# Kernel tuning notes

Hardware: AMD Instinct MI355X
Metric: run time of the kernel (lower is better)

The kernel has to match this reference:

```python
import jax, jax.numpy as jnp
import numpy as np

WS = 14          # window size
NH = 12          # num heads
C = 768          # hidden dim
HD = C // NH     # head dim = 64
MLP = 3072       # mlp dim
EPS = 1e-6


def _layernorm(x, g, b):
    mu = jnp.mean(x, axis=-1, keepdims=True)
    var = jnp.mean(jnp.square(x - mu), axis=-1, keepdims=True)
    return (x - mu) * jax.lax.rsqrt(var + EPS) * g + b


def setup_inputs() -> dict:
    key = jax.random.key(0)
    ks = jax.random.split(key, 8)
    B, H, W = 8, 64, 64
    f32 = jnp.float32
    d = {}
    d["x"] = jax.random.normal(ks[0], (B, H, W, C), f32)
    d["ln1_g"] = jnp.ones((C,), f32)
    d["ln1_b"] = jnp.zeros((C,), f32)
    d["qkv_w"] = (jax.random.normal(ks[1], (C, 3 * C), f32) * 0.02)
    d["qkv_b"] = jnp.zeros((3 * C,), f32)
    d["proj_w"] = (jax.random.normal(ks[2], (C, C), f32) * 0.02)
    d["proj_b"] = jnp.zeros((C,), f32)
    d["rel_pos_h"] = (jax.random.normal(ks[3], (2 * WS - 1, HD), f32) * 0.02)
    d["rel_pos_w"] = (jax.random.normal(ks[4], (2 * WS - 1, HD), f32) * 0.02)
    d["ln2_g"] = jnp.ones((C,), f32)
    d["ln2_b"] = jnp.zeros((C,), f32)
    d["mlp_w1"] = (jax.random.normal(ks[5], (C, MLP), f32) * 0.02)
    d["mlp_b1"] = jnp.zeros((MLP,), f32)
    d["mlp_w2"] = (jax.random.normal(ks[6], (MLP, C), f32) * 0.02)
    d["mlp_b2"] = jnp.zeros((C,), f32)
    return d


def reference(x, ln1_g, ln1_b, qkv_w, qkv_b, proj_w, proj_b,
              rel_pos_h, rel_pos_w, ln2_g, ln2_b,
              mlp_w1, mlp_b1, mlp_w2, mlp_b2):
    B, H, W, _ = x.shape
    xn = _layernorm(x, ln1_g, ln1_b)

    # ---- window partition (pad to multiple of WS) ----
    pad_h = (-H) % WS
    pad_w = (-W) % WS
    Hp, Wp = H + pad_h, W + pad_w
    xp = jnp.pad(xn, ((0, 0), (0, pad_h), (0, pad_w), (0, 0)))
    # [B, Hp/WS, WS, Wp/WS, WS, C] -> [Bn, WS, WS, C]
    win = xp.reshape(B, Hp // WS, WS, Wp // WS, WS, C)
    win = win.transpose(0, 1, 3, 2, 4, 5).reshape(-1, WS, WS, C)
    Bn = win.shape[0]
    N = WS * WS

    # ---- attention with decomposed relative position bias ----
    qkv = win.reshape(Bn, N, C) @ qkv_w + qkv_b                 # [Bn, N, 3C]
    qkv = qkv.reshape(Bn, N, 3, NH, HD).transpose(2, 0, 3, 1, 4)
    qkv = qkv.reshape(3, Bn * NH, N, HD)
    q, k, v = qkv[0], qkv[1], qkv[2]

    scale = HD ** -0.5
    attn = jnp.einsum('bnd,bmd->bnm', q * scale, k)             # [Bn*NH, N, N]

    # rel coords: q_size == k_size == WS, rel_pos already has 2*WS-1 rows
    coords = jnp.arange(WS)[:, None] - jnp.arange(WS)[None, :] + (WS - 1)
    Rh = rel_pos_h[coords]                                      # [WS, WS, HD]
    Rw = rel_pos_w[coords]                                      # [WS, WS, HD]
    rq = q.reshape(Bn * NH, WS, WS, HD)
    rel_h = jnp.einsum('bhwc,hkc->bhwk', rq, Rh)                # [B', WS, WS, WS]
    rel_w = jnp.einsum('bhwc,wkc->bhwk', rq, Rw)
    attn = (attn.reshape(Bn * NH, WS, WS, WS, WS)
            + rel_h[:, :, :, :, None]
            + rel_w[:, :, :, None, :]).reshape(Bn * NH, N, N)

    attn = jax.nn.softmax(attn, axis=-1)
    out = jnp.einsum('bnm,bmd->bnd', attn, v)                   # [Bn*NH, N, HD]
    out = out.reshape(Bn, NH, WS, WS, HD).transpose(0, 2, 3, 1, 4).reshape(Bn, WS, WS, C)
    out = out @ proj_w + proj_b

    # ---- window unpartition ----
    out = out.reshape(B, Hp // WS, Wp // WS, WS, WS, C)
    out = out.transpose(0, 1, 3, 2, 4, 5).reshape(B, Hp, Wp, C)[:, :H, :W, :]

    x1 = x + out
    y = _layernorm(x1, ln2_g, ln2_b)
    y = jax.nn.gelu(y @ mlp_w1 + mlp_b1, approximate=False) @ mlp_w2 + mlp_b2
    return x1 + y
```

## Files before the change

kernel.cpp:

```cpp
#include <hip/hip_runtime.h>
#include <hip/hip_bf16.h>
#include <cstdint>
#include <cstddef>

using bf16 = __hip_bfloat16;
typedef __attribute__((ext_vector_type(8))) short short8;
typedef __attribute__((ext_vector_type(4))) float f32x4;

typedef __attribute__((address_space(1))) const void as1_void;
typedef __attribute__((address_space(3))) void as3_void;

__device__ __forceinline__ f32x4 mfma16x16x32(short8 a, short8 b, f32x4 c) {
  return __builtin_amdgcn_mfma_f32_16x16x32_bf16(a, b, c, 0, 0, 0);
}

__device__ __forceinline__ void gload_lds16(const void* g, void* l) {
  __builtin_amdgcn_global_load_lds((as1_void*)g, (as3_void*)l, 16, 0, 0);
}

__device__ __forceinline__ uint32_t cvtpk(float a, float b) {
  uint32_t r;
  asm("v_cvt_pk_bf16_f32 %0, %1, %2" : "=v"(r) : "v"(a), "v"(b));
  return r;
}

__device__ __forceinline__ void vmwait4() { asm volatile("s_waitcnt vmcnt(4)" ::: "memory"); }
__device__ __forceinline__ void vmwait0() { asm volatile("s_waitcnt vmcnt(0)" ::: "memory"); }

__device__ __forceinline__ float gelu_f(float v) {
  const float u = 0.7978845608f * v * (1.f + 0.044715f * v * v);
  const float e = __expf(-2.f * fabsf(u));
  const float t = (1.f - e) / (1.f + e);
  return 0.5f * v * (1.f + (u < 0.f ? -t : t));
}

static constexpr int MROWS = 39200;
static constexpr int MPAD  = 39296;
static constexpr int TOK2  = 32768;

__global__ __launch_bounds__(256)
void transpose_cast(const float* __restrict__ in, bf16* __restrict__ out, int K, int N) {
  __shared__ float t[32][33];
  const int tx = threadIdx.x & 31, ty = threadIdx.x >> 5;
  const int bx = blockIdx.x, by = blockIdx.y;
  const int x = bx * 32 + tx;
  for (int r = ty; r < 32; r += 8)
    t[r][tx] = in[(size_t)(by * 32 + r) * N + x];
  __syncthreads();
  const int xo = by * 32 + tx;
  for (int r = ty; r < 32; r += 8)
    out[(size_t)(bx * 32 + r) * K + xo] = __float2bfloat16(t[tx][r]);
}

__global__ __launch_bounds__(256)
void ln1_partition(const float* __restrict__ x, const float* __restrict__ g,
                   const float* __restrict__ bb, bf16* __restrict__ out) {
  const int token = blockIdx.x * 4 + (threadIdx.x >> 6);
  const int lane = threadIdx.x & 63;
  const int win = token / 196, tok = token % 196;
  const int b_ = win / 25, wh = (win / 5) % 5, ww = win % 5;
  const int i = tok / 14, j = tok % 14;
  const int h = wh * 14 + i, w = ww * 14 + j;
  bf16* o = out + (size_t)token * 768;
  if (h >= 64 || w >= 64) {
    for (int t = 0; t < 12; ++t) o[lane + 64 * t] = __float2bfloat16(0.f);
    return;
  }
  const float* src = x + ((size_t)((b_ * 64 + h) * 64 + w)) * 768;
  float vals[12], s = 0.f, ss = 0.f;
  #pragma unroll
  for (int t = 0; t < 12; ++t) {
    float v = src[lane + 64 * t];
    vals[t] = v; s += v; ss += v * v;
  }
  #pragma unroll
  for (int d = 32; d > 0; d >>= 1) { s += __shfl_xor(s, d); ss += __shfl_xor(ss, d); }
  const float mu = s * (1.f / 768.f);
  const float var = ss * (1.f / 768.f) - mu * mu;
  const float inv = rsqrtf(var + 1e-6f);
  #pragma unroll
  for (int t = 0; t < 12; ++t) {
    const int c = lane + 64 * t;
    o[c] = __float2bfloat16((vals[t] - mu) * inv * g[c] + bb[c]);
  }
}

__global__ __launch_bounds__(256)
void ln2_kernel(const float* __restrict__ x1, const float* __restrict__ g,
                const float* __restrict__ bb, bf16* __restrict__ out) {
  const int token = blockIdx.x * 4 + (threadIdx.x >> 6);
  const int lane = threadIdx.x & 63;
  const float* src = x1 + (size_t)token * 768;
  bf16* o = out + (size_t)token * 768;
  float vals[12], s = 0.f, ss = 0.f;
  #pragma unroll
  for (int t = 0; t < 12; ++t) {
    float v = src[lane + 64 * t];
    vals[t] = v; s += v; ss += v * v;
  }
  #pragma unroll
  for (int d = 32; d > 0; d >>= 1) { s += __shfl_xor(s, d); ss += __shfl_xor(ss, d); }
  const float mu = s * (1.f / 768.f);
  const float var = ss * (1.f / 768.f) - mu * mu;
  const float inv = rsqrtf(var + 1e-6f);
  #pragma unroll
  for (int t = 0; t < 12; ++t) {
    const int c = lane + 64 * t;
    o[c] = __float2bfloat16((vals[t] - mu) * inv * g[c] + bb[c]);
  }
}

template<int EPI>
__global__ __launch_bounds__(256)
void gemm_bf16(const bf16* __restrict__ A, const bf16* __restrict__ Bt,
               const float* __restrict__ bias, int K, int Mreal,
               const float* __restrict__ fin, float* __restrict__ fout,
               bf16* __restrict__ ob0, bf16* __restrict__ ob1, bf16* __restrict__ ob2) {
  __shared__ __align__(16) bf16 SMEM[16384];
  bf16* const lA0 = SMEM;
  bf16* const lA1 = SMEM + 4096;
  bf16* const lB0 = SMEM + 8192;
  bf16* const lB1 = SMEM + 12288;
  const int tid = threadIdx.x;
  const int lane = tid & 63, wv = tid >> 6;
  const int lr = lane & 15, hi = lane >> 4;
  const int wm = wv >> 1, wn = wv & 1;

  const int gx = gridDim.x;
  const int nwg = gx * gridDim.y;
  int lin = blockIdx.y * gx + blockIdx.x;
  {
    const int q8 = nwg >> 3, r8 = nwg & 7;
    const int xcd = lin & 7, pos = lin >> 3;
    lin = (xcd < r8 ? xcd * (q8 + 1) : r8 * (q8 + 1) + (xcd - r8) * q8) + pos;
  }
  const size_t arow0 = (size_t)(lin / gx) * 128;
  const size_t brow0 = (size_t)(lin % gx) * 128;
  f32x4 acc[4][4] = {};

  auto stage = [&](bf16* bufA, bf16* bufB, int kt) {
    const int k0 = kt * 32;
    #pragma unroll
    for (int it = 0; it < 2; ++it) {
      const int seg = it * 256 + tid;
      const int row = seg >> 2, kq = seg & 3;
      const size_t dst = (size_t)(it * 256 + wv * 64) * 8;
      if constexpr (EPI == 1) {
        const int k = k0 + kq * 8;
        gload_lds16(A + ((size_t)(k >> 6) * MPAD + arow0 + row) * 64 + (k & 63), bufA + dst);
      } else {
        gload_lds16(A + (arow0 + row) * K + k0 + kq * 8, bufA + dst);
      }
      gload_lds16(Bt + (brow0 + row) * K + k0 + kq * 8, bufB + dst);
    }
  };
  auto compute = [&](const bf16* bufA, const bf16* bufB) {
    short8 af[4], bfr[4];
    #pragma unroll
    for (int m = 0; m < 4; ++m) af[m] = *(const short8*)&bufA[(wm * 64 + m * 16 + lr) * 32 + hi * 8];
    #pragma unroll
    for (int n = 0; n < 4; ++n) bfr[n] = *(const short8*)&bufB[(wn * 64 + n * 16 + lr) * 32 + hi * 8];
    #pragma unroll
    for (int m = 0; m < 4; ++m)
      #pragma unroll
      for (int n = 0; n < 4; ++n)
        acc[m][n] = mfma16x16x32(af[m], bfr[n], acc[m][n]);
  };

  const int nt = K >> 5;
  stage(lA0, lB0, 0);
  stage(lA1, lB1, 1);
  for (int t = 0; t < nt; t += 2) {
    vmwait4();
    __builtin_amdgcn_s_barrier();
    __builtin_amdgcn_sched_barrier(0);
    compute(lA0, lB0);
    __builtin_amdgcn_sched_barrier(0);
    __builtin_amdgcn_s_barrier();
    if (t + 2 < nt) { stage(lA0, lB0, t + 2); vmwait4(); }
    else            { vmwait0(); }
    __builtin_amdgcn_s_barrier();
    __builtin_amdgcn_sched_barrier(0);
    compute(lA1, lB1);
    __builtin_amdgcn_sched_barrier(0);
    __builtin_amdgcn_s_barrier();
    if (t + 3 < nt) stage(lA1, lB1, t + 3);
  }

  if constexpr (EPI == 0 || EPI == 2) {
    bf16* ct = SMEM;
    #pragma unroll
    for (int n = 0; n < 4; ++n) {
      const int col = wn * 64 + n * 16 + lr;
      const float bv = bias[(int)brow0 + col];
      #pragma unroll
      for (int m = 0; m < 4; ++m) {
        #pragma unroll
        for (int e = 0; e < 4; ++e) {
          const int row = wm * 64 + m * 16 + hi * 4 + e;
          float v = acc[m][n][e] + bv;
          if constexpr (EPI == 2) v = gelu_f(v);
          const int byte = (row << 8) + (col << 1);
          *(bf16*)((char*)ct + (byte ^ ((row & 7) << 5))) = __float2bfloat16(v);
        }
      }
    }
    __syncthreads();
    #pragma unroll
    for (int i = 0; i < 8; ++i) {
      const int lin16 = i * 256 + tid;
      const int row = lin16 >> 4;
      const int u   = lin16 & 15;
      const int byte = (row << 8) + (u << 4);
      const short8 val = *(const short8*)((char*)ct + (byte ^ ((row & 7) << 5)));
      const int grow = (int)arow0 + row;
      const int gcol = (int)brow0 + u * 8;
      if constexpr (EPI == 0) {
        if (grow < Mreal) {
          const int which = gcol / 768, head = (gcol >> 6) % 12, d = gcol & 63;
          bf16* dstb = (which == 0) ? ob0 : ((which == 1) ? ob1 : ob2);
          *(short8*)&dstb[((size_t)head * MPAD + grow) * 64 + d] = val;
        }
      } else {
        *(short8*)&ob0[(size_t)grow * 3072 + gcol] = val;
      }
    }
  } else {
    #pragma unroll
    for (int n = 0; n < 4; ++n) {
      const int col = (int)brow0 + wn * 64 + n * 16 + lr;
      const float bv = bias[col];
      #pragma unroll
      for (int m = 0; m < 4; ++m) {
        #pragma unroll
        for (int e = 0; e < 4; ++e) {
          const int row = (int)arow0 + wm * 64 + m * 16 + hi * 4 + e;
          const float v = acc[m][n][e] + bv;
          if constexpr (EPI == 1) {
            if (row < Mreal) {
              const int win = row / 196, tok = row % 196;
              const int b_ = win / 25, wh = (win / 5) % 5, ww = win % 5;
              const int i = tok / 14, j = tok % 14;
              const int h = wh * 14 + i, w = ww * 14 + j;
              if (h < 64 && w < 64) {
                const size_t idx = ((size_t)((b_ * 64 + h) * 64 + w)) * 768 + col;
                fout[idx] = fin[idx] + v;
              }
            }
          } else {
            const size_t idx = (size_t)row * 768 + col;
            fout[idx] = fin[idx] + v;
          }
        }
      }
    }
  }
}

__global__ __launch_bounds__(256)
void attn_kernel(const bf16* __restrict__ qb, const bf16* __restrict__ kb,
                 const bf16* __restrict__ vb, const float* __restrict__ rph,
                 const float* __restrict__ rpw, bf16* __restrict__ aout) {
  __shared__ __align__(16) char SM[65248];
  bf16* pbh    = (bf16*)SM;
  bf16* pbw    = (bf16*)(SM + 4096);
  bf16* Gh     = (bf16*)(SM + 8192);
  bf16* Gw     = (bf16*)(SM + 23168);
  char* klds   = SM;
  char* vtb    = SM + 25600;
  bf16* relh_s = (bf16*)(SM + 54272);
  bf16* relw_s = (bf16*)(SM + 59760);

  const int bh = blockIdx.x;
  const int win = bh / 12, head = bh % 12;
  const size_t base = ((size_t)head * MPAD + win * 196) * 64;
  const bf16* Q  = qb + base;
  const bf16* Kp = kb + base;
  const bf16* Vp = vb + base;
  const int tid = threadIdx.x, lane = tid & 63, wv = tid >> 6;
  const int lr = lane & 15, hi = lane >> 4;

  for (int i = tid; i < 32 * 64; i += 256) {
    const int r = i >> 6, c = i & 63;
    const bool ok = r < 27;
    pbh[i] = __float2bfloat16(ok ? rph[r * 64 + c] : 0.f);
    pbw[i] = __float2bfloat16(ok ? rpw[r * 64 + c] : 0.f);
  }
  __syncthreads();
  {
    short8 bh00 = *(const short8*)&pbh[(lr) * 64 + hi * 8];
    short8 bh01 = *(const short8*)&pbh[(lr) * 64 + 32 + hi * 8];
    short8 bh10 = *(const short8*)&pbh[(16 + lr) * 64 + hi * 8];
    short8 bh11 = *(const short8*)&pbh[(16 + lr) * 64 + 32 + hi * 8];
    short8 bw00 = *(const short8*)&pbw[(lr) * 64 + hi * 8];
    short8 bw01 = *(const short8*)&pbw[(lr) * 64 + 32 + hi * 8];
    short8 bw10 = *(const short8*)&pbw[(16 + lr) * 64 + hi * 8];
    short8 bw11 = *(const short8*)&pbw[(16 + lr) * 64 + 32 + hi * 8];
    for (int mt = wv; mt < 13; mt += 4) {
      const short8 a0 = *(const short8*)&Q[(mt * 16 + lr) * 64 + hi * 8];
      const short8 a1 = *(const short8*)&Q[(mt * 16 + lr) * 64 + 32 + hi * 8];
      f32x4 g0 = {}, g1 = {}, g2 = {}, g3 = {};
      g0 = mfma16x16x32(a0, bh00, g0); g0 = mfma16x16x32(a1, bh01, g0);
      g1 = mfma16x16x32(a0, bh10, g1); g1 = mfma16x16x32(a1, bh11, g1);
      g2 = mfma16x16x32(a0, bw00, g2); g2 = mfma16x16x32(a1, bw01, g2);
      g3 = mfma16x16x32(a0, bw10, g3); g3 = mfma16x16x32(a1, bw11, g3);
      #pragma unroll
      for (int e = 0; e < 4; ++e) {
        const int row = mt * 16 + hi * 4 + e;
        Gh[row * 36 + lr]      = __float2bfloat16(g0[e]);
        Gh[row * 36 + 16 + lr] = __float2bfloat16(g1[e]);
        Gw[row * 36 + lr]      = __float2bfloat16(g2[e]);
        Gw[row * 36 + 16 + lr] = __float2bfloat16(g3[e]);
      }
    }
  }
  __syncthreads();
  bf16 ghr[11], gwr[11];
  #pragma unroll
  for (int t = 0; t < 11; ++t) {
    const int i = tid + t * 256;
    if (i < 196 * 14) {
      const int q = i / 14, kk = i - (i / 14) * 14;
      const int rh = q / 14 - kk + 13;
      const int rw2 = q - (q / 14) * 14 - kk + 13;
      ghr[t] = Gh[q * 36 + rh];
      gwr[t] = Gw[q * 36 + rw2];
    }
  }
  __syncthreads();
  #pragma unroll
  for (int t = 0; t < 11; ++t) {
    const int i = tid + t * 256;
    if (i < 196 * 14) { relh_s[i] = ghr[t]; relw_s[i] = gwr[t]; }
  }
  for (int c = wv; c < 25; c += 4) {
    const int row = c * 8 + (lane >> 3);
    const int ch  = (lane & 7) ^ (row & 7);
    gload_lds16(Kp + row * 64 + ch * 8, klds + c * 1024);
  }
  for (int i = tid; i < 196 * 8; i += 256) {
    const int key = i >> 3, dg = (i & 7) * 8;
    const short8 v = *(const short8*)&Vp[key * 64 + dg];
    #pragma unroll
    for (int j = 0; j < 8; ++j) {
      const int idx = (dg + j) * 448 + key * 2;
      *(bf16*)(vtb + (idx ^ (j << 4))) = ((const bf16*)&v)[j];
    }
  }
  for (int i = tid; i < 64 * 28; i += 256) {
    const int d = i / 28, key = 196 + i - (i / 28) * 28;
    const int idx = d * 448 + key * 2;
    *(bf16*)(vtb + (idx ^ ((d & 7) << 4))) = __float2bfloat16(0.f);
  }
  __syncthreads();

  for (int qt = wv; qt < 13; qt += 4) {
    const int q = qt * 16 + lr;
    const int qc = q < 196 ? q : 195;
    const short8 bq0 = *(const short8*)&Q[(qt * 16 + lr) * 64 + hi * 8];
    const short8 bq1 = *(const short8*)&Q[(qt * 16 + lr) * 64 + 32 + hi * 8];
    f32x4 s[13];
    __builtin_amdgcn_s_setprio(1);
    #pragma unroll
    for (int nt = 0; nt < 13; ++nt) {
      const int key = nt * 16 + lr;
      const char* kr = klds + key * 128;
      const short8 ka0 = *(const short8*)(kr + (((hi) ^ (key & 7)) << 4));
      const short8 ka1 = *(const short8*)(kr + (((hi + 4) ^ (key & 7)) << 4));
      f32x4 z = {};
      z = mfma16x16x32(ka0, bq0, z);
      z = mfma16x16x32(ka1, bq1, z);
      s[nt] = z;
    }
    __builtin_amdgcn_s_setprio(0);
    float mx = -3.0e38f;
    #pragma unroll
    for (int nt = 0; nt < 13; ++nt) {
      #pragma unroll
      for (int e = 0; e < 4; ++e) {
        const int key = nt * 16 + hi * 4 + e;
        const int kh = key / 14, kw = key - kh * 14;
        float v = s[nt][e] * 0.125f + __bfloat162float(relh_s[qc * 14 + kh])
                                    + __bfloat162float(relw_s[qc * 14 + kw]);
        v = (key < 196) ? v : -3.0e38f;
        s[nt][e] = v;
        mx = fmaxf(mx, v);
      }
    }
    mx = fmaxf(mx, __shfl_xor(mx, 16));
    mx = fmaxf(mx, __shfl_xor(mx, 32));
    float sm = 0.f;
    #pragma unroll
    for (int nt = 0; nt < 13; ++nt)
      #pragma unroll
      for (int e = 0; e < 4; ++e) {
        const float p = __expf(s[nt][e] - mx);
        s[nt][e] = p; sm += p;
      }
    sm += __shfl_xor(sm, 16);
    sm += __shfl_xor(sm, 32);
    const float rinv = 1.f / sm;
    f32x4 o[4] = {};
    #pragma unroll
    for (int kk = 0; kk < 7; ++kk) {
      const uint32_t x0 = cvtpk(s[2 * kk][0] * rinv, s[2 * kk][1] * rinv);
      const uint32_t x1 = cvtpk(s[2 * kk][2] * rinv, s[2 * kk][3] * rinv);
      const uint32_t y0 = cvtpk(s[2 * kk + 1][0] * rinv, s[2 * kk + 1][1] * rinv);
      const uint32_t y1 = cvtpk(s[2 * kk + 1][2] * rinv, s[2 * kk + 1][3] * rinv);
      const uint32_t s0 = (hi < 2) ? y0 : x0, s1 = (hi < 2) ? y1 : x1;
      const uint32_t t0 = __shfl_xor(s0, 32), t1 = __shfl_xor(s1, 32);
      const uint32_t o0 = (hi < 2) ? x0 : y0, o1 = (hi < 2) ? x1 : y1;
      const bool sendOwn = (hi == 1) || (hi == 2);
      const uint32_t u0 = sendOwn ? o0 : t0, u1 = sendOwn ? o1 : t1;
      const uint32_t r0 = __shfl_xor(u0, 16), r1 = __shfl_xor(u1, 16);
      union { uint32_t u[4]; short8 v; } pf;
      pf.u[0] = (hi == 0) ? x0 : ((hi == 2) ? t0 : r0);
      pf.u[1] = (hi == 0) ? x1 : ((hi == 2) ? t1 : r1);
      pf.u[2] = (hi == 3) ? y0 : ((hi == 1) ? t0 : r0);
      pf.u[3] = (hi == 3) ? y1 : ((hi == 1) ? t1 : r1);
      __builtin_amdgcn_s_setprio(1);
      #pragma unroll
      for (int n2 = 0; n2 < 4; ++n2) {
        const int d = n2 * 16 + lr;
        const int idx = d * 448 + (kk * 32 + hi * 8) * 2;
        const short8 va = *(const short8*)(vtb + (idx ^ ((lr & 7) << 4)));
        o[n2] = mfma16x16x32(va, pf.v, o[n2]);
      }
      __builtin_amdgcn_s_setprio(0);
    }
    if (q < 196) {
      bf16* orow = aout + ((size_t)head * MPAD + win * 196 + q) * 64;
      #pragma unroll
      for (int n2 = 0; n2 < 4; ++n2) {
        uint32_t d0 = cvtpk(o[n2][0], o[n2][1]);
        uint32_t d1 = cvtpk(o[n2][2], o[n2][3]);
        uint32_t* dst = (uint32_t*)&orow[n2 * 16 + hi * 4];
        dst[0] = d0; dst[1] = d1;
      }
    }
  }
}

extern "C" void kernel_launch(void* const* d_in, const int* in_sizes, int n_in,
                              void* d_out, int out_size, void* d_ws, size_t ws_size,
                              hipStream_t stream) {
  (void)in_sizes; (void)n_in; (void)out_size; (void)ws_size;
  const float* x      = (const float*)d_in[0];
  const float* ln1_g  = (const float*)d_in[1];
  const float* ln1_b  = (const float*)d_in[2];
  const float* qkv_w  = (const float*)d_in[3];
  const float* qkv_b  = (const float*)d_in[4];
  const float* proj_w = (const float*)d_in[5];
  const float* proj_b = (const float*)d_in[6];
  const float* rph    = (const float*)d_in[7];
  const float* rpw    = (const float*)d_in[8];
  const float* ln2_g  = (const float*)d_in[9];
  const float* ln2_b  = (const float*)d_in[10];
  const float* w1     = (const float*)d_in[11];
  const float* b1v    = (const float*)d_in[12];
  const float* w2     = (const float*)d_in[13];
  const float* b2v    = (const float*)d_in[14];
  float* outp = (float*)d_out;

  char* ws = (char*)d_ws;
  size_t off = 0;
  auto alloc = [&](size_t bytes) { char* p = ws + off; off += (bytes + 255) & ~(size_t)255; return p; };
  bf16* qkv_wt  = (bf16*)alloc((size_t)2304 * 768 * 2);
  bf16* proj_wt = (bf16*)alloc((size_t)768 * 768 * 2);
  bf16* w1t     = (bf16*)alloc((size_t)3072 * 768 * 2);
  bf16* w2t     = (bf16*)alloc((size_t)768 * 3072 * 2);
  const size_t szB1 = (size_t)MPAD * 768 * 2;
  const size_t szB2 = (size_t)TOK2 * 768 * 2;
  char* regB = alloc(szB1 > szB2 ? szB1 : szB2);
  const size_t szQKV = (size_t)3 * 12 * MPAD * 64 * 2;
  const size_t szH   = (size_t)TOK2 * 3072 * 2;
  char* regC = alloc(szQKV > szH ? szQKV : szH);

  bf16* xnwin   = (bf16*)regB;
  bf16* attnout = (bf16*)regB;
  bf16* xn2     = (bf16*)regB;
  bf16* qbuf    = (bf16*)regC;
  bf16* kbuf    = qbuf + (size_t)12 * MPAD * 64;
  bf16* vbuf    = kbuf + (size_t)12 * MPAD * 64;
  bf16* hbuf    = (bf16*)regC;

  transpose_cast<<<dim3(2304 / 32, 768 / 32), 256, 0, stream>>>(qkv_w, qkv_wt, 768, 2304);
  transpose_cast<<<dim3(768 / 32, 768 / 32), 256, 0, stream>>>(proj_w, proj_wt, 768, 768);
  transpose_cast<<<dim3(3072 / 32, 768 / 32), 256, 0, stream>>>(w1, w1t, 768, 3072);
  transpose_cast<<<dim3(768 / 32, 3072 / 32), 256, 0, stream>>>(w2, w2t, 3072, 768);

  ln1_partition<<<dim3(MROWS / 4), 256, 0, stream>>>(x, ln1_g, ln1_b, xnwin);

  gemm_bf16<0><<<dim3(2304 / 128, MPAD / 128), 256, 0, stream>>>(
      xnwin, qkv_wt, qkv_b, 768, MROWS, nullptr, nullptr, qbuf, kbuf, vbuf);

  attn_kernel<<<dim3(2400), 256, 0, stream>>>(qbuf, kbuf, vbuf, rph, rpw, attnout);

  gemm_bf16<1><<<dim3(768 / 128, MPAD / 128), 256, 0, stream>>>(
      attnout, proj_wt, proj_b, 768, MROWS, x, outp, nullptr, nullptr, nullptr);

  ln2_kernel<<<dim3(TOK2 / 4), 256, 0, stream>>>(outp, ln2_g, ln2_b, xn2);

  gemm_bf16<2><<<dim3(3072 / 128, TOK2 / 128), 256, 0, stream>>>(
      xn2, w1t, b1v, 768, TOK2, nullptr, nullptr, hbuf, nullptr, nullptr);
  gemm_bf16<3><<<dim3(768 / 128, TOK2 / 128), 256, 0, stream>>>(
      hbuf, w2t, b2v, 3072, TOK2, outp, outp, nullptr, nullptr, nullptr);
}
```

Baseline: 1.140 ms.

## Write V transposed from QKV GEMM and read K/V directly in attention

The QKV GEMM epilogue now writes V in a head-major, d-major (transposed) layout. The attention kernel therefore drops its LDS staging of K and the LDS transpose of V, and reads both straight from global memory. That cuts attention LDS use and raises the occupancy hint to 3 blocks per CU, at the cost of uncoalesced per-lane global reads inside the MFMA loops. Separately, the GEMM main loop replaces the hand-scheduled double-buffer waits and barriers with a simpler stage-ahead pattern using __syncthreads. That may reduce how well loads overlap with MFMA work.

```diff
diff --git a/kernel.cpp b/kernel.cpp
--- a/kernel.cpp
+++ b/kernel.cpp
@@ -23,9 +23,6 @@
   asm("v_cvt_pk_bf16_f32 %0, %1, %2" : "=v"(r) : "v"(a), "v"(b));
   return r;
 }
-
-__device__ __forceinline__ void vmwait4() { asm volatile("s_waitcnt vmcnt(4)" ::: "memory"); }
-__device__ __forceinline__ void vmwait0() { asm volatile("s_waitcnt vmcnt(0)" ::: "memory"); }
 
 __device__ __forceinline__ float gelu_f(float v) {
   const float u = 0.7978845608f * v * (1.f + 0.044715f * v * v);
@@ -169,22 +166,14 @@
 
   const int nt = K >> 5;
   stage(lA0, lB0, 0);
-  stage(lA1, lB1, 1);
+  __syncthreads();
   for (int t = 0; t < nt; t += 2) {
-    vmwait4();
-    __builtin_amdgcn_s_barrier();
-    __builtin_amdgcn_sched_barrier(0);
+    if (t + 1 < nt) stage(lA1, lB1, t + 1);
     compute(lA0, lB0);
-    __builtin_amdgcn_sched_barrier(0);
-    __builtin_amdgcn_s_barrier();
-    if (t + 2 < nt) { stage(lA0, lB0, t + 2); vmwait4(); }
-    else            { vmwait0(); }
-    __builtin_amdgcn_s_barrier();
-    __builtin_amdgcn_sched_barrier(0);
+    __syncthreads();
+    if (t + 2 < nt) stage(lA0, lB0, t + 2);
     compute(lA1, lB1);
-    __builtin_amdgcn_sched_barrier(0);
-    __builtin_amdgcn_s_barrier();
-    if (t + 3 < nt) stage(lA1, lB1, t + 3);
+    __syncthreads();
   }
 
   if constexpr (EPI == 0 || EPI == 2) {
@@ -206,23 +195,50 @@
       }
     }
     __syncthreads();
-    #pragma unroll
-    for (int i = 0; i < 8; ++i) {
-      const int lin16 = i * 256 + tid;
-      const int row = lin16 >> 4;
-      const int u   = lin16 & 15;
-      const int byte = (row << 8) + (u << 4);
-      const short8 val = *(const short8*)((char*)ct + (byte ^ ((row & 7) << 5)));
-      const int grow = (int)arow0 + row;
-      const int gcol = (int)brow0 + u * 8;
-      if constexpr (EPI == 0) {
-        if (grow < Mreal) {
-          const int which = gcol / 768, head = (gcol >> 6) % 12, d = gcol & 63;
-          bf16* dstb = (which == 0) ? ob0 : ((which == 1) ? ob1 : ob2);
-          *(short8*)&dstb[((size_t)head * MPAD + grow) * 64 + d] = val;
+    if constexpr (EPI == 0) {
+      if ((int)brow0 >= 1536) {
+        const int head_base = ((int)brow0 >> 6) % 12;
+        #pragma unroll
+        for (int i = 0; i < 8; ++i) {
+          const int idx = i * 256 + tid;
+          const int dl = idx >> 4;
+          const int h2 = dl >> 6, d = dl & 63;
+          const int tg = (idx & 15) * 8;
+          union { bf16 h[8]; short8 v; } u8;
+          #pragma unroll
+          for (int j = 0; j < 8; ++j) {
+            const int tok = tg + j;
+            const int byte = (tok << 8) + (dl << 1);
+            u8.h[j] = *(const bf16*)((const char*)ct + (byte ^ ((tok & 7) << 5)));
+          }
+          *(short8*)&ob2[((size_t)(head_base + h2) * 64 + d) * MPAD + arow0 + tg] = u8.v;
         }
       } else {
-        *(short8*)&ob0[(size_t)grow * 3072 + gcol] = val;
+        #pragma unroll
+        for (int i = 0; i < 8; ++i) {
+          const int lin16 = i * 256 + tid;
+          const int row = lin16 >> 4;
+          const int u   = lin16 & 15;
+          const int byte = (row << 8) + (u << 4);
+          const short8 val = *(const short8*)((char*)ct + (byte ^ ((row & 7) << 5)));
+          const int grow = (int)arow0 + row;
+          const int gcol = (int)brow0 + u * 8;
+          if (grow < Mreal) {
+            const int which = gcol / 768, head = (gcol >> 6) % 12, d = gcol & 63;
+            bf16* dstb = (which == 0) ? ob0 : ob1;
+            *(short8*)&dstb[((size_t)head * MPAD + grow) * 64 + d] = val;
+          }
+        }
+      }
+    } else {
+      #pragma unroll
+      for (int i = 0; i < 8; ++i) {
+        const int lin16 = i * 256 + tid;
+        const int row = lin16 >> 4;
+        const int u   = lin16 & 15;
+        const int byte = (row << 8) + (u << 4);
+        const short8 val = *(const short8*)((char*)ct + (byte ^ ((row & 7) << 5)));
+        *(short8*)&ob0[(size_t)((int)arow0 + row) * 3072 + (int)brow0 + u * 8] = val;
       }
     }
   } else {
@@ -257,26 +273,24 @@
   }
 }
 
-__global__ __launch_bounds__(256)
+__global__ __launch_bounds__(256, 3)
 void attn_kernel(const bf16* __restrict__ qb, const bf16* __restrict__ kb,
-                 const bf16* __restrict__ vb, const float* __restrict__ rph,
+                 const bf16* __restrict__ vtg_all, const float* __restrict__ rph,
                  const float* __restrict__ rpw, bf16* __restrict__ aout) {
-  __shared__ __align__(16) char SM[65248];
+  __shared__ __align__(16) char SM[38144];
   bf16* pbh    = (bf16*)SM;
   bf16* pbw    = (bf16*)(SM + 4096);
   bf16* Gh     = (bf16*)(SM + 8192);
   bf16* Gw     = (bf16*)(SM + 23168);
-  char* klds   = SM;
-  char* vtb    = SM + 25600;
-  bf16* relh_s = (bf16*)(SM + 54272);
-  bf16* relw_s = (bf16*)(SM + 59760);
+  bf16* relh_s = (bf16*)SM;
+  bf16* relw_s = (bf16*)(SM + 5488);
 
   const int bh = blockIdx.x;
   const int win = bh / 12, head = bh % 12;
   const size_t base = ((size_t)head * MPAD + win * 196) * 64;
-  const bf16* Q  = qb + base;
-  const bf16* Kp = kb + base;
-  const bf16* Vp = vb + base;
+  const bf16* Q   = qb + base;
+  const bf16* Kp  = kb + base;
+  const bf16* Vt  = vtg_all + (size_t)head * 64 * MPAD + win * 196;
   const int tid = threadIdx.x, lane = tid & 63, wv = tid >> 6;
   const int lr = lane & 15, hi = lane >> 4;
 
@@ -333,25 +347,6 @@
     const int i = tid + t * 256;
     if (i < 196 * 14) { relh_s[i] = ghr[t]; relw_s[i] = gwr[t]; }
   }
-  for (int c = wv; c < 25; c += 4) {
-    const int row = c * 8 + (lane >> 3);
-    const int ch  = (lane & 7) ^ (row & 7);
-    gload_lds16(Kp + row * 64 + ch * 8, klds + c * 1024);
-  }
-  for (int i = tid; i < 196 * 8; i += 256) {
-    const int key = i >> 3, dg = (i & 7) * 8;
-    const short8 v = *(const short8*)&Vp[key * 64 + dg];
-    #pragma unroll
-    for (int j = 0; j < 8; ++j) {
-      const int idx = (dg + j) * 448 + key * 2;
-      *(bf16*)(vtb + (idx ^ (j << 4))) = ((const bf16*)&v)[j];
-    }
-  }
-  for (int i = tid; i < 64 * 28; i += 256) {
-    const int d = i / 28, key = 196 + i - (i / 28) * 28;
-    const int idx = d * 448 + key * 2;
-    *(bf16*)(vtb + (idx ^ ((d & 7) << 4))) = __float2bfloat16(0.f);
-  }
   __syncthreads();
 
   for (int qt = wv; qt < 13; qt += 4) {
@@ -359,14 +354,13 @@
     const int qc = q < 196 ? q : 195;
     const short8 bq0 = *(const short8*)&Q[(qt * 16 + lr) * 64 + hi * 8];
     const short8 bq1 = *(const short8*)&Q[(qt * 16 + lr) * 64 + 32 + hi * 8];
-    f32x4 s[13];
+    f32x4 s[14];
     __builtin_amdgcn_s_setprio(1);
     #pragma unroll
     for (int nt = 0; nt < 13; ++nt) {
       const int key = nt * 16 + lr;
-      const char* kr = klds + key * 128;
-      const short8 ka0 = *(const short8*)(kr + (((hi) ^ (key & 7)) << 4));
-      const short8 ka1 = *(const short8*)(kr + (((hi + 4) ^ (key & 7)) << 4));
+      const short8 ka0 = *(const short8*)&Kp[key * 64 + hi * 8];
+      const short8 ka1 = *(const short8*)&Kp[key * 64 + 32 + hi * 8];
       f32x4 z = {};
       z = mfma16x16x32(ka0, bq0, z);
       z = mfma16x16x32(ka1, bq1, z);
@@ -400,6 +394,7 @@
     sm += __shfl_xor(sm, 16);
     sm += __shfl_xor(sm, 32);
     const float rinv = 1.f / sm;
+    s[13] = f32x4{0.f, 0.f, 0.f, 0.f};
     f32x4 o[4] = {};
     #pragma unroll
     for (int kk = 0; kk < 7; ++kk) {
@@ -422,8 +417,7 @@
       #pragma unroll
       for (int n2 = 0; n2 < 4; ++n2) {
         const int d = n2 * 16 + lr;
-        const int idx = d * 448 + (kk * 32 + hi * 8) * 2;
-        const short8 va = *(const short8*)(vtb + (idx ^ ((lr & 7) << 4)));
+        const short8 va = *(const short8*)&Vt[(size_t)d * MPAD + kk * 32 + hi * 8];
         o[n2] = mfma16x16x32(va, pf.v, o[n2]);
       }
       __builtin_amdgcn_s_setprio(0);
@@ -481,7 +475,7 @@
   bf16* xn2     = (bf16*)regB;
   bf16* qbuf    = (bf16*)regC;
   bf16* kbuf    = qbuf + (size_t)12 * MPAD * 64;
-  bf16* vbuf    = kbuf + (size_t)12 * MPAD * 64;
+  bf16* vbuf_t  = kbuf + (size_t)12 * MPAD * 64;
   bf16* hbuf    = (bf16*)regC;
 
   transpose_cast<<<dim3(2304 / 32, 768 / 32), 256, 0, stream>>>(qkv_w, qkv_wt, 768, 2304);
@@ -492,9 +486,9 @@
   ln1_partition<<<dim3(MROWS / 4), 256, 0, stream>>>(x, ln1_g, ln1_b, xnwin);
 
   gemm_bf16<0><<<dim3(2304 / 128, MPAD / 128), 256, 0, stream>>>(
-      xnwin, qkv_wt, qkv_b, 768, MROWS, nullptr, nullptr, qbuf, kbuf, vbuf);
-
-  attn_kernel<<<dim3(2400), 256, 0, stream>>>(qbuf, kbuf, vbuf, rph, rpw, attnout);
+      xnwin, qkv_wt, qkv_b, 768, MROWS, nullptr, nullptr, qbuf, kbuf, vbuf_t);
+
+  attn_kernel<<<dim3(2400), 256, 0, stream>>>(qbuf, kbuf, vbuf_t, rph, rpw, attnout);
 
   gemm_bf16<1><<<dim3(768 / 128, MPAD / 128), 256, 0, stream>>>(
       attnout, proj_wt, proj_b, 768, MROWS, x, outp, nullptr, nullptr, nullptr);
```

Result: slower. 1.342 ms (+17.7%).
